# Kernel tuning notes

Measured on AMD Instinct MI355X. Metric: run time of the kernel, lower is better.

## Reference

```python
import jax, jax.numpy as jnp
import numpy as np
from jax import lax

ANCHOR_SCALES = (64.0, 128.0, 256.0)
ANCHOR_RATIOS = (0.5, 1.0, 2.0)
STRIDE = 32
NMS_THRESH = 0.7


def make_anchors(feat_h, feat_w):
    base = []
    for s in ANCHOR_SCALES:
        for r in ANCHOR_RATIOS:
            w = s * np.sqrt(max(r, 1e-6))
            h = s / np.sqrt(max(r, 1e-6))
            base.append([-w / 2, -h / 2, w / 2, h / 2])
    base = jnp.asarray(base, jnp.float32)  # [A=9, 4]
    sx = jnp.arange(feat_w, dtype=jnp.float32) * STRIDE
    sy = jnp.arange(feat_h, dtype=jnp.float32) * STRIDE
    yy, xx = jnp.meshgrid(sy, sx, indexing='ij')
    shifts = jnp.stack([xx, yy, xx, yy], axis=2).reshape(-1, 4)  # [H*W, 4]
    # location-major, anchor-minor -> matches permute(0,2,3,1).view(B,-1,·)
    return (base[None, :, :] + shifts[:, None, :]).reshape(-1, 4)  # [N, 4]


def apply_deltas(anchors, deltas):
    w = anchors[:, 2] - anchors[:, 0]
    h = anchors[:, 3] - anchors[:, 1]
    cx = anchors[:, 0] + 0.5 * w
    cy = anchors[:, 1] + 0.5 * h
    pcx = deltas[:, 0] * w + cx
    pcy = deltas[:, 1] * h + cy
    pw = jnp.exp(deltas[:, 2]) * w
    ph = jnp.exp(deltas[:, 3]) * h
    return jnp.stack([pcx - 0.5 * pw, pcy - 0.5 * ph,
                      pcx + 0.5 * pw, pcy + 0.5 * ph], axis=1)


def pairwise_iou(b):
    area = (b[:, 2] - b[:, 0]) * (b[:, 3] - b[:, 1])
    lt = jnp.maximum(b[:, None, :2], b[None, :, :2])
    rb = jnp.minimum(b[:, None, 2:], b[None, :, 2:])
    wh = jnp.clip(rb - lt, 0.0)
    inter = wh[..., 0] * wh[..., 1]
    return inter / (area[:, None] + area[None, :] - inter)


def nms_keep(boxes, scores, thresh):
    # greedy NMS (torchvision semantics: suppress iou > thresh), returns bool keep mask
    n = boxes.shape[0]
    order = jnp.argsort(-scores)
    sb = boxes[order]
    idx = jnp.arange(n)
    sup_mat = (pairwise_iou(sb) > thresh) & (idx[None, :] > idx[:, None])

    def body(i, sup):
        return sup | ((~sup[i]) & sup_mat[i])

    sup = lax.fori_loop(0, n, body, jnp.zeros(n, bool))
    return jnp.zeros(n, bool).at[order].set(~sup)


def setup_inputs() -> dict:
    key = jax.random.key(0)
    ks = jax.random.split(key, 4)
    features = jax.random.normal(ks[0], (4, 512, 25, 25), jnp.float32)
    conv_w = jax.random.normal(ks[1], (512, 512, 3, 3), jnp.float32) * 0.01
    conv_b = jnp.zeros((512,), jnp.float32)
    cls_w = jax.random.normal(ks[2], (18, 512), jnp.float32) * 0.01
    cls_b = jnp.zeros((18,), jnp.float32)
    bbox_w = jax.random.normal(ks[3], (36, 512), jnp.float32) * 0.01
    bbox_b = jnp.zeros((36,), jnp.float32)
    return {"features": features, "conv_w": conv_w, "conv_b": conv_b,
            "cls_w": cls_w, "cls_b": cls_b, "bbox_w": bbox_w, "bbox_b": bbox_b,
            "img_h": 800, "img_w": 800}


def reference(features, conv_w, conv_b, cls_w, cls_b, bbox_w, bbox_b, img_h, img_w):
    B, _, H, W = features.shape
    x = lax.conv_general_dilated(features, conv_w, (1, 1), 'SAME',
                                 dimension_numbers=('NCHW', 'OIHW', 'NCHW'))
    x = jax.nn.relu(x + conv_b[None, :, None, None])
    obj = jnp.einsum('bchw,oc->bohw', x, cls_w) + cls_b[None, :, None, None]
    dlt = jnp.einsum('bchw,oc->bohw', x, bbox_w) + bbox_b[None, :, None, None]
    obj = obj.transpose(0, 2, 3, 1).reshape(B, -1, 2)      # [B, N, 2]
    dlt = dlt.transpose(0, 2, 3, 1).reshape(B, -1, 4)      # [B, N, 4]

    anchors = make_anchors(H, W)                            # [N, 4]
    props = jax.vmap(lambda d: apply_deltas(anchors, d))(dlt)
    hi = jnp.asarray([img_w, img_h, img_w, img_h], jnp.float32)
    props = jnp.clip(props, 0.0, hi)                        # clip to image
    scores = jax.nn.softmax(obj, axis=-1)[..., 1]           # [B, N]
    keep = jax.vmap(lambda b, s: nms_keep(b, s, NMS_THRESH))(props, scores)
    # suppressed boxes zeroed (fixed-shape analogue of props[keep])
    return props * keep[..., None].astype(props.dtype)
```

## Files before the change

kernel.cpp:

```cpp
#include <hip/hip_runtime.h>


#define NBATCH 4
#define HWDIM  25
#define NPOS   625
#define NM     2500
#define CIN    512
#define NANCH  5625
#define NW     88
#define CAP    4096

typedef unsigned long long u64;
typedef unsigned int u32;

struct BaseAnchors { float x1[9], y1[9], x2[9], y2[9]; };

__device__ __forceinline__ u64 bcast64(u64 v, int lane) {
  unsigned int lo = (unsigned int)v;
  unsigned int hi = (unsigned int)(v >> 32);
  lo = (unsigned int)__builtin_amdgcn_readlane((int)lo, lane);
  hi = (unsigned int)__builtin_amdgcn_readlane((int)hi, lane);
  return (((u64)hi) << 32) | (u64)lo;
}

__device__ __forceinline__ u64 waveOr64(u64 x) {
  unsigned int lo = (unsigned int)x, hi = (unsigned int)(x >> 32);
#pragma unroll
  for (int off = 32; off > 0; off >>= 1) {
    lo |= (unsigned int)__shfl_xor((int)lo, off, 64);
    hi |= (unsigned int)__shfl_xor((int)hi, off, 64);
  }
  return (((u64)hi) << 32) | (u64)lo;
}


__global__ void transpose_features(const float* __restrict__ f, float* __restrict__ fm) {
  __shared__ float tile[32][33];
  int b  = blockIdx.z;
  int p0 = blockIdx.x * 32;
  int c0 = blockIdx.y * 32;
  int tx = threadIdx.x, ty = threadIdx.y;
#pragma unroll
  for (int j = 0; j < 4; j++) {
    int c = c0 + ty + j * 8;
    int p = p0 + tx;
    if (p < NPOS) tile[ty + j * 8][tx] = f[((size_t)(b * CIN + c)) * NPOS + p];
  }
  __syncthreads();
#pragma unroll
  for (int j = 0; j < 4; j++) {
    int p = p0 + ty + j * 8;
    int c = c0 + tx;
    if (p < NPOS) fm[((size_t)(b * NPOS + p)) * CIN + c] = tile[tx][ty + j * 8];
  }
}

__global__ __launch_bounds__(256) void transpose_weights(const float* __restrict__ cw,
                                                         float* __restrict__ Wt) {
  __shared__ float tile[32][289];
  int o0 = blockIdx.x * 32, c0 = blockIdx.y * 32;
  int tid = threadIdx.x;
#pragma unroll
  for (int j = 0; j < 36; j++) {
    int idx = tid + j * 256;
    int o = idx / 288, kk = idx % 288;
    tile[o][kk] = cw[((size_t)(o0 + o)) * 4608 + c0 * 9 + kk];
  }
  __syncthreads();
  int ol = tid & 31, pg = tid >> 5;
#pragma unroll
  for (int j = 0; j < 36; j++) {
    int pair = pg + j * 8;
    int c = pair / 9, tap = pair % 9;
    Wt[((size_t)tap * CIN + (c0 + c)) * 512 + o0 + ol] = tile[ol][pair];
  }
}

__global__ void build_wco(const float* __restrict__ clsw, const float* __restrict__ clsb,
                          const float* __restrict__ bw, const float* __restrict__ bbb,
                          float* __restrict__ Wco, float* __restrict__ bco) {
  int idx = blockIdx.x * 256 + threadIdx.x;
  if (idx < 512 * 64) {
    int c = idx >> 6, o = idx & 63;
    float v = 0.f;
    if (o < 18) v = clsw[o * 512 + c];
    else if (o < 54) v = bw[(o - 18) * 512 + c];
    Wco[idx] = v;
  }
  if (idx < 64) {
    float v = 0.f;
    if (idx < 18) v = clsb[idx];
    else if (idx < 54) v = bbb[idx - 18];
    bco[idx] = v;
  }
}

__global__ void zero_cnt(u32* __restrict__ cnt) {
  int i = blockIdx.x * 64 + threadIdx.x;
  if (i < NBATCH * NW) cnt[i] = 0u;
}

__global__ __launch_bounds__(256) void conv_gemm(const float* __restrict__ fm,
                                                 const float* __restrict__ Wt,
                                                 float* __restrict__ xp) {
  __shared__ __align__(16) float At[32][68];
  __shared__ __align__(16) float Bt[32][64];
  int tid = threadIdx.x;
  int m0 = blockIdx.x << 6;
  int o0 = blockIdx.y << 6;
  int part = blockIdx.z;
  int ti = tid >> 4, tj = tid & 15;
  int si = tid >> 2, sq = tid & 3;
  int skk = tid >> 3, sr = tid & 7;
  float acc[4][4] = {{0.f}};

  int m = m0 + si;
  bool mv = m < NM;
  int mm = mv ? m : 0;
  int bb = mm / NPOS, rem = mm % NPOS;
  int hh = rem / HWDIM, ww = rem % HWDIM;
  int dy = part - 1;

  for (int tt = 0; tt < 3; tt++) {
    int tap = part * 3 + tt;
    int dx = tt - 1;
    int h2 = hh + dy, w2 = ww + dx;
    bool av = mv && ((unsigned)h2 < (unsigned)HWDIM) && ((unsigned)w2 < (unsigned)HWDIM);
    const float* arow = fm + (((size_t)(bb * NPOS + h2 * HWDIM + w2)) << 9);
    const float* bbase = Wt + (((size_t)tap) << 18) + o0;

    float4 a0 = make_float4(0.f, 0.f, 0.f, 0.f), a1 = a0;
    if (av) {
      a0 = *(const float4*)(arow + (sq << 2));
      a1 = *(const float4*)(arow + 16 + (sq << 2));
    }
    const float* bp0 = bbase + (((size_t)skk) << 9);
    float4 b0 = *(const float4*)(bp0 + (sr << 2));
    float4 b1 = *(const float4*)(bp0 + 32 + (sr << 2));

    for (int c0 = 0; c0 < CIN; c0 += 32) {
      __syncthreads();
      int kb = sq << 2;
      At[kb + 0][si] = a0.x; At[kb + 1][si] = a0.y; At[kb + 2][si] = a0.z; At[kb + 3][si] = a0.w;
      At[kb + 16][si] = a1.x; At[kb + 17][si] = a1.y; At[kb + 18][si] = a1.z; At[kb + 19][si] = a1.w;
      *(float4*)&Bt[skk][sr << 2] = b0;
      *(float4*)&Bt[skk][32 + (sr << 2)] = b1;
      float4 na0 = make_float4(0.f, 0.f, 0.f, 0.f), na1 = na0;
      float4 nb0 = na0, nb1 = na0;
      int c1 = c0 + 32;
      if (c1 < CIN) {
        if (av) {
          na0 = *(const float4*)(arow + c1 + (sq << 2));
          na1 = *(const float4*)(arow + c1 + 16 + (sq << 2));
        }
        const float* bp = bbase + (((size_t)(c1 + skk)) << 9);
        nb0 = *(const float4*)(bp + (sr << 2));
        nb1 = *(const float4*)(bp + 32 + (sr << 2));
      }
      __syncthreads();
#pragma unroll
      for (int kk = 0; kk < 32; kk++) {
        float4 avv = *(const float4*)&At[kk][ti << 2];
        float4 bvv = *(const float4*)&Bt[kk][tj << 2];
        float a_[4] = {avv.x, avv.y, avv.z, avv.w};
        float b_[4] = {bvv.x, bvv.y, bvv.z, bvv.w};
#pragma unroll
        for (int u = 0; u < 4; u++)
#pragma unroll
          for (int v = 0; v < 4; v++) acc[u][v] += a_[u] * b_[v];
      }
      a0 = na0; a1 = na1; b0 = nb0; b1 = nb1;
    }
  }
  float* outp = xp + (size_t)part * (NM * 512);
#pragma unroll
  for (int u = 0; u < 4; u++) {
    int mr = m0 + (ti << 2) + u;
    if (mr < NM) {
      float4 r = make_float4(acc[u][0], acc[u][1], acc[u][2], acc[u][3]);
      *(float4*)(outp + (((size_t)mr) << 9) + o0 + (tj << 2)) = r;
    }
  }
}

__global__ void combine_relu(const float* __restrict__ xp, const float* __restrict__ bias,
                             float* __restrict__ x2) {
  int i4 = blockIdx.x * 256 + threadIdx.x;
  if (i4 >= NM * 128) return;
  float4 p0 = *(const float4*)(xp + (size_t)i4 * 4);
  float4 p1 = *(const float4*)(xp + (size_t)(NM * 512) + (size_t)i4 * 4);
  float4 p2 = *(const float4*)(xp + (size_t)(2 * NM * 512) + (size_t)i4 * 4);
  float4 bb = *(const float4*)(bias + (i4 & 127) * 4);
  float4 r;
  r.x = fmaxf(p0.x + p1.x + p2.x + bb.x, 0.f);
  r.y = fmaxf(p0.y + p1.y + p2.y + bb.y, 0.f);
  r.z = fmaxf(p0.z + p1.z + p2.z + bb.z, 0.f);
  r.w = fmaxf(p0.w + p1.w + p2.w + bb.w, 0.f);
  *(float4*)(x2 + (size_t)i4 * 4) = r;
}

__global__ __launch_bounds__(256) void gemm1x1(const float* __restrict__ x2,
                                               const float* __restrict__ Wco,
                                               const float* __restrict__ bco,
                                               float* __restrict__ logits) {
  __shared__ __align__(16) float At[32][68];
  __shared__ __align__(16) float Bt[32][64];
  int tid = threadIdx.x;
  int m0 = blockIdx.x << 6;
  int ti = tid >> 4, tj = tid & 15;
  int si = tid >> 2, sq = tid & 3;
  int skk = tid >> 3, sr = tid & 7;
  float acc[4][4] = {{0.f}};
  int m = m0 + si;
  bool mv = m < NM;
  const float* arow = x2 + (((size_t)(mv ? m : 0)) << 9);
  for (int c0 = 0; c0 < CIN; c0 += 32) {
    __syncthreads();
    float4 a0 = make_float4(0.f, 0.f, 0.f, 0.f), a1 = a0;
    if (mv) {
      a0 = *(const float4*)(arow + c0 + (sq << 2));
      a1 = *(const float4*)(arow + c0 + 16 + (sq << 2));
    }
    int kb = sq << 2;
    At[kb + 0][si] = a0.x; At[kb + 1][si] = a0.y; At[kb + 2][si] = a0.z; At[kb + 3][si] = a0.w;
    At[kb + 16][si] = a1.x; At[kb + 17][si] = a1.y; At[kb + 18][si] = a1.z; At[kb + 19][si] = a1.w;
    const float* bp = Wco + (size_t)(c0 + skk) * 64;
    *(float4*)&Bt[skk][sr << 2] = *(const float4*)(bp + (sr << 2));
    *(float4*)&Bt[skk][32 + (sr << 2)] = *(const float4*)(bp + 32 + (sr << 2));
    __syncthreads();
#pragma unroll
    for (int kk = 0; kk < 32; kk++) {
      float4 avv = *(const float4*)&At[kk][ti << 2];
      float4 bvv = *(const float4*)&Bt[kk][tj << 2];
      float a_[4] = {avv.x, avv.y, avv.z, avv.w};
      float b_[4] = {bvv.x, bvv.y, bvv.z, bvv.w};
#pragma unroll
      for (int u = 0; u < 4; u++)
#pragma unroll
        for (int v = 0; v < 4; v++) acc[u][v] += a_[u] * b_[v];
    }
  }
  float4 bias = *(const float4*)(bco + (tj << 2));
#pragma unroll
  for (int u = 0; u < 4; u++) {
    int mr = m0 + (ti << 2) + u;
    if (mr < NM) {
      float4 r = make_float4(acc[u][0] + bias.x, acc[u][1] + bias.y, acc[u][2] + bias.z,
                             acc[u][3] + bias.w);
      *(float4*)(logits + (size_t)mr * 64 + (tj << 2)) = r;
    }
  }
}

__global__ __launch_bounds__(256) void score_box_kernel(const float* __restrict__ logits,
                                                        const int* __restrict__ ih,
                                                        const int* __restrict__ iw,
                                                        BaseAnchors ba,
                                                        float* __restrict__ scores,
                                                        float* __restrict__ props) {
#pragma clang fp contract(off)
  int n = blockIdx.x * 256 + threadIdx.x;
  if (n >= NBATCH * NANCH) return;
  int b = n / NANCH;
  int r = n % NANCH;
  int pos = r / 9, aa = r % 9;
  int py = pos / HWDIM, px = pos % HWDIM;
  const float* L = logits + (size_t)(b * NPOS + pos) * 64;
  float l0 = L[2 * aa], l1 = L[2 * aa + 1];
  float mx = fmaxf(l0, l1);
  float e0 = expf(l0 - mx), e1 = expf(l1 - mx);
  float s = e1 / (e0 + e1);
  float d0 = L[18 + 4 * aa + 0], d1 = L[18 + 4 * aa + 1];
  float d2 = L[18 + 4 * aa + 2], d3 = L[18 + 4 * aa + 3];
  float xf = (float)px * 32.f, yf = (float)py * 32.f;
  float ax1 = ba.x1[aa] + xf, ay1 = ba.y1[aa] + yf;
  float ax2 = ba.x2[aa] + xf, ay2 = ba.y2[aa] + yf;
  float wA = ax2 - ax1, hA = ay2 - ay1;
  float cx = ax1 + 0.5f * wA, cy = ay1 + 0.5f * hA;
  float pcx = d0 * wA + cx, pcy = d1 * hA + cy;
  float pw = expf(d2) * wA, ph = expf(d3) * hA;
  float x1 = pcx - 0.5f * pw, y1 = pcy - 0.5f * ph;
  float x2 = pcx + 0.5f * pw, y2 = pcy + 0.5f * ph;
  float W = (float)iw[0], H = (float)ih[0];
  x1 = fminf(fmaxf(x1, 0.f), W);
  y1 = fminf(fmaxf(y1, 0.f), H);
  x2 = fminf(fmaxf(x2, 0.f), W);
  y2 = fminf(fmaxf(y2, 0.f), H);
  scores[n] = s;
  *(float4*)(props + (size_t)n * 4) = make_float4(x1, y1, x2, y2);
}

__global__ __launch_bounds__(1024) void sort_kernel(const float* __restrict__ scores,
                                                    const float* __restrict__ props,
                                                    int* __restrict__ order,
                                                    float* __restrict__ sb) {
  __shared__ u64 keys[8192];
  int b = blockIdx.x, tid = threadIdx.x;
  const float* sc = scores + (size_t)b * NANCH;
  for (int i = tid; i < 8192; i += 1024) {
    u64 k = 0ull;
    if (i < NANCH) {
      unsigned int sbits = __float_as_uint(sc[i]);
      k = (((u64)sbits) << 32) | (u64)(~(unsigned int)i);
    }
    keys[i] = k;
  }
  __syncthreads();
  for (int k = 2; k <= 8192; k <<= 1) {
    for (int j = k >> 1; j > 0; j >>= 1) {
#pragma unroll
      for (int s = 0; s < 8; s++) {
        int i = tid + (s << 10);
        int p = i ^ j;
        if (p > i) {
          u64 a = keys[i], c = keys[p];
          bool up = ((i & k) == 0);
          bool sw = up ? (a < c) : (a > c);
          if (sw) { keys[i] = c; keys[p] = a; }
        }
      }
      __syncthreads();
    }
  }
  for (int i = tid; i < NANCH; i += 1024) {
    u64 kk = keys[i];
    int orig = (int)(~(unsigned int)kk);
    order[b * NANCH + i] = orig;
    float4 p = *(const float4*)(props + ((size_t)b * NANCH + orig) * 4);
    *(float4*)(sb + ((size_t)b * NANCH + i) * 4) = p;
  }
}

__global__ __launch_bounds__(64) void nms_mask_kernel(const float* __restrict__ sb,
                                                      uint4* __restrict__ lists,
                                                      u32* __restrict__ cnt,
                                                      u64* __restrict__ maskd) {
#pragma clang fp contract(off)
  int rb = blockIdx.x, cb = blockIdx.y, b = blockIdx.z;
  if (cb < rb) return;
  int lane = threadIdx.x;
  __shared__ float4 cbox[64];
  int j0 = cb << 6;
  const float* sbb = sb + (size_t)b * NANCH * 4;
  if (j0 + lane < NANCH) cbox[lane] = *(const float4*)(sbb + (size_t)(j0 + lane) * 4);
  __syncthreads();
  int i = (rb << 6) + lane;
  if (i >= NANCH) return;
  float4 rbox = *(const float4*)(sbb + (size_t)i * 4);
  float rarea = (rbox.z - rbox.x) * (rbox.w - rbox.y);
  u64 bits = 0ull;
  int jmax = NANCH - j0;
  if (jmax > 64) jmax = 64;
  for (int l = 0; l < jmax; l++) {
    int j = j0 + l;
    if (j > i) {
      float4 c = cbox[l];
      float carea = (c.z - c.x) * (c.w - c.y);
      float ltx = fmaxf(rbox.x, c.x), lty = fmaxf(rbox.y, c.y);
      float rbx = fminf(rbox.z, c.z), rby = fminf(rbox.w, c.w);
      float wx = fmaxf(rbx - ltx, 0.f);
      float wy = fmaxf(rby - lty, 0.f);
      float inter = wx * wy;
      float iou = inter / (rarea + carea - inter);
      if (iou > 0.7f) bits |= (1ull << l);
    }
  }
  if (rb == cb) {
    maskd[((size_t)b * NW + rb) * 64 + lane] = bits;
  } else if (bits) {
    u32 idx = atomicAdd(&cnt[b * NW + cb], 1u);
    if (idx < CAP)
      lists[((size_t)(b * NW + cb)) * CAP + idx] =
          make_uint4((u32)bits, (u32)(bits >> 32), (u32)i, 0u);
  }
}

__global__ __launch_bounds__(64, 1) void nms_scan_kernel(const uint4* __restrict__ lists,
                                                         const u32* __restrict__ cnt,
                                                         const u64* __restrict__ maskd,
                                                         const int* __restrict__ order,
                                                         const float* __restrict__ sb,
                                                         float* __restrict__ out) {
  int b = blockIdx.x;
  int lane = threadIdx.x;
  __shared__ u64 keep_sh[NW];
  const u64* md = maskd + (size_t)b * NW * 64;
  const uint4* lb = lists + (size_t)b * NW * CAP;

  u32 c0 = (lane < NW) ? cnt[b * NW + lane] : 0u;
  u32 c1 = (lane + 64 < NW) ? cnt[b * NW + lane + 64] : 0u;

  u64 diag = md[lane];
  uint4 pf = lb[lane];
  for (int s = 0; s < NW; s++) {
    u64 Mw = diag;
    uint4 e0 = pf;
    if (s + 1 < NW) {
      diag = md[((s + 1) << 6) + lane];
      pf = lb[(size_t)(s + 1) * CAP + lane];
    }

    int cn = (int)(u32)__builtin_amdgcn_readlane(
        (int)((s < 64) ? c0 : c1), (s < 64) ? s : s - 64);
    if (cn > CAP) cn = CAP;

    u64 acc = 0ull;
    if (lane < cn) {
      u64 kw = keep_sh[e0.z >> 6];
      if ((kw >> (e0.z & 63)) & 1ull) acc |= (((u64)e0.y) << 32) | (u64)e0.x;
    }
    for (int p = lane + 64; p < cn; p += 64) {
      uint4 e = lb[(size_t)s * CAP + p];
      u64 kw = keep_sh[e.z >> 6];
      if ((kw >> (e.z & 63)) & 1ull) acc |= (((u64)e.y) << 32) | (u64)e.x;
    }
    u64 cur = waveOr64(acc);

    int nrows = NANCH - (s << 6);
    if (nrows > 64) nrows = 64;
    u64 valid = (nrows < 64) ? ((1ull << nrows) - 1ull) : ~0ull;

    u64 nz = __ballot(Mw != 0ull);
    u64 todo = nz & ~cur & valid;
    while (todo) {
      int t = (int)__builtin_ctzll(todo);
      cur |= bcast64(Mw, t);
      todo &= ~cur;
      todo &= ~(1ull << t);
    }
    u64 alive = (~cur) & valid;
    if (lane == 0) keep_sh[s] = alive;
  }

  for (int i = lane; i < NANCH; i += 64) {
    u64 kw = keep_sh[i >> 6];
    bool kept = ((kw >> (i & 63)) & 1ull) != 0ull;
    int orig = order[b * NANCH + i];
    float4 p = *(const float4*)(sb + ((size_t)b * NANCH + i) * 4);
    float4 o = kept ? p : make_float4(0.f, 0.f, 0.f, 0.f);
    *(float4*)(out + ((size_t)b * NANCH + orig) * 4) = o;
  }
}


extern "C" void kernel_launch(void* const* d_in, const int* in_sizes, int n_in,
                              void* d_out, int out_size, void* d_ws, size_t ws_size,
                              hipStream_t stream) {
  const float* features = (const float*)d_in[0];
  const float* conv_w   = (const float*)d_in[1];
  const float* conv_b   = (const float*)d_in[2];
  const float* cls_w    = (const float*)d_in[3];
  const float* cls_b    = (const float*)d_in[4];
  const float* bbox_w   = (const float*)d_in[5];
  const float* bbox_b   = (const float*)d_in[6];
  const int*   img_h    = (const int*)d_in[7];
  const int*   img_w    = (const int*)d_in[8];
  float* out = (float*)d_out;
  char* ws = (char*)d_ws;

  const size_t OFF_FM    = 0;
  const size_t OFF_WT    = 5120000;
  const size_t OFF_XP    = 14557184;
  const size_t OFF_LISTS = 0;
  const size_t OFF_CNT   = 23068672;
  const size_t OFF_MASKD = 23070208;
  const size_t OFF_X2  = 29917184;
  const size_t OFF_WCO = 35037184;
  const size_t OFF_BCO = 35168256;
  const size_t OFF_LOG = 35168512;
  const size_t OFF_SC  = 35808512;
  const size_t OFF_PR  = 35898512;
  const size_t OFF_ORD = 36258512;
  const size_t OFF_SB  = 36348512;
  const size_t WS_NEEDED = 36708512;
  if (ws_size < WS_NEEDED) return;

  float* fm   = (float*)(ws + OFF_FM);
  float* Wt   = (float*)(ws + OFF_WT);
  float* xp   = (float*)(ws + OFF_XP);
  uint4* lists = (uint4*)(ws + OFF_LISTS);
  u32*   cnt   = (u32*)(ws + OFF_CNT);
  u64*   maskd = (u64*)(ws + OFF_MASKD);
  float* x2   = (float*)(ws + OFF_X2);
  float* Wco  = (float*)(ws + OFF_WCO);
  float* bco  = (float*)(ws + OFF_BCO);
  float* logits = (float*)(ws + OFF_LOG);
  float* scores = (float*)(ws + OFF_SC);
  float* props  = (float*)(ws + OFF_PR);
  int*   order  = (int*)(ws + OFF_ORD);
  float* sb     = (float*)(ws + OFF_SB);

  BaseAnchors ba;
  {
    const double scales[3] = {64.0, 128.0, 256.0};
    const double ratios[3] = {0.5, 1.0, 2.0};
    int a = 0;
    for (int si = 0; si < 3; si++)
      for (int ri = 0; ri < 3; ri++, a++) {
        double w = scales[si] * sqrt(ratios[ri]);
        double h = scales[si] / sqrt(ratios[ri]);
        ba.x1[a] = (float)(-w / 2.0);
        ba.y1[a] = (float)(-h / 2.0);
        ba.x2[a] = (float)(w / 2.0);
        ba.y2[a] = (float)(h / 2.0);
      }
  }

  transpose_features<<<dim3(20, 16, 4), dim3(32, 8), 0, stream>>>(features, fm);
  transpose_weights<<<dim3(16, 16), 256, 0, stream>>>(conv_w, Wt);
  build_wco<<<128, 256, 0, stream>>>(cls_w, cls_b, bbox_w, bbox_b, Wco, bco);
  conv_gemm<<<dim3(40, 8, 3), 256, 0, stream>>>(fm, Wt, xp);
  combine_relu<<<1250, 256, 0, stream>>>(xp, conv_b, x2);
  gemm1x1<<<40, 256, 0, stream>>>(x2, Wco, bco, logits);
  score_box_kernel<<<88, 256, 0, stream>>>(logits, img_h, img_w, ba, scores, props);
  sort_kernel<<<4, 1024, 0, stream>>>(scores, props, order, sb);
  zero_cnt<<<6, 64, 0, stream>>>(cnt);
  nms_mask_kernel<<<dim3(NW, NW, 4), 64, 0, stream>>>(sb, lists, cnt, maskd);
  nms_scan_kernel<<<4, 64, 0, stream>>>(lists, cnt, maskd, order, sb, out);
}
```

Measured before the change: 457.5 us.

## Replace bitonic sort with stable LSD radix sort in shared memory

Swaps the 8192-element 64-bit-key bitonic sort for a 4-pass, 8-bit-digit LSD radix sort over 32-bit score keys with separate index values. Per-wave histograms, a block prefix scan and ballot-based match ranking give a stable descending order, so index tie-breaking is preserved. The goal is to cut the roughly 91 barrier-separated bitonic stages down to a few dozen barriers. In exchange it uses more LDS, which limits occupancy, and adds scan overhead.

Result: faster. 390.0 us (-14.7%).

```diff
diff --git a/kernel.cpp b/kernel.cpp
--- a/kernel.cpp
+++ b/kernel.cpp
@@ -9,6 +9,7 @@
 #define NANCH  5625
 #define NW     88
 #define CAP    4096
+#define SORTN  6144
 
 typedef unsigned long long u64;
 typedef unsigned int u32;
@@ -290,43 +291,89 @@
   *(float4*)(props + (size_t)n * 4) = make_float4(x1, y1, x2, y2);
 }
 
-__global__ __launch_bounds__(1024) void sort_kernel(const float* __restrict__ scores,
-                                                    const float* __restrict__ props,
-                                                    int* __restrict__ order,
-                                                    float* __restrict__ sb) {
-  __shared__ u64 keys[8192];
+__global__ __launch_bounds__(1024, 1) void radix_sort_kernel(const float* __restrict__ scores,
+                                                             const float* __restrict__ props,
+                                                             int* __restrict__ order,
+                                                             float* __restrict__ sb) {
+  __shared__ u32 kA[SORTN], vA[SORTN], kB[SORTN], vB[SORTN];
+  __shared__ u32 hist[16][256];
+  __shared__ u32 tot[256], base[256], tmp[256];
   int b = blockIdx.x, tid = threadIdx.x;
+  int lane = tid & 63, wv = tid >> 6;
   const float* sc = scores + (size_t)b * NANCH;
-  for (int i = tid; i < 8192; i += 1024) {
-    u64 k = 0ull;
-    if (i < NANCH) {
-      unsigned int sbits = __float_as_uint(sc[i]);
-      k = (((u64)sbits) << 32) | (u64)(~(unsigned int)i);
-    }
-    keys[i] = k;
+
+  for (int i = tid; i < SORTN; i += 1024) {
+    kA[i] = (i < NANCH) ? __float_as_uint(sc[i]) : 0u;
+    vA[i] = (u32)i;
   }
   __syncthreads();
-  for (int k = 2; k <= 8192; k <<= 1) {
-    for (int j = k >> 1; j > 0; j >>= 1) {
-#pragma unroll
-      for (int s = 0; s < 8; s++) {
-        int i = tid + (s << 10);
-        int p = i ^ j;
-        if (p > i) {
-          u64 a = keys[i], c = keys[p];
-          bool up = ((i & k) == 0);
-          bool sw = up ? (a < c) : (a > c);
-          if (sw) { keys[i] = c; keys[p] = a; }
-        }
+
+  for (int pass = 0; pass < 4; pass++) {
+    int shift = pass << 3;
+    u32* ks = (pass & 1) ? kB : kA;
+    u32* vs = (pass & 1) ? vB : vA;
+    u32* kd = (pass & 1) ? kA : kB;
+    u32* vd = (pass & 1) ? vA : vB;
+    for (int i = tid; i < 4096; i += 1024) ((u32*)hist)[i] = 0u;
+    __syncthreads();
+    for (int r = 0; r < 6; r++) {
+      int i = wv * 384 + (r << 6) + lane;
+      u32 d = 255u - ((ks[i] >> shift) & 255u);
+      atomicAdd(&hist[wv][d], 1u);
+    }
+    __syncthreads();
+    if (tid < 256) {
+      u32 run = 0;
+#pragma unroll
+      for (int w = 0; w < 16; w++) { u32 t = hist[w][tid]; hist[w][tid] = run; run += t; }
+      tot[tid] = run;
+    }
+    __syncthreads();
+    if (tid < 256) tmp[tid] = tot[tid];
+    __syncthreads();
+    for (int off = 1; off < 256; off <<= 1) {
+      u32 v = 0;
+      if (tid < 256 && tid >= off) v = tmp[tid - off];
+      __syncthreads();
+      if (tid < 256) tmp[tid] += v;
+      __syncthreads();
+    }
+    if (tid < 256) base[tid] = tmp[tid] - tot[tid];
+    __syncthreads();
+    if (tid < 256) {
+      u32 bs = base[tid];
+#pragma unroll
+      for (int w = 0; w < 16; w++) hist[w][tid] += bs;
+    }
+    __syncthreads();
+    for (int r = 0; r < 6; r++) {
+      int i = wv * 384 + (r << 6) + lane;
+      u32 key = ks[i], val = vs[i];
+      u32 d = 255u - ((key >> shift) & 255u);
+      u64 grp = ~0ull;
+#pragma unroll
+      for (int bit = 0; bit < 8; bit++) {
+        u64 bal = __ballot(((d >> bit) & 1u) != 0u);
+        grp &= ((d >> bit) & 1u) ? bal : ~bal;
       }
-      __syncthreads();
-    }
-  }
+      u64 ltmask = (1ull << lane) - 1ull;
+      u32 rank = (u32)__popcll(grp & ltmask);
+      int leader = (int)__builtin_ctzll(grp);
+      u32 oldv = 0;
+      if (lane == leader) oldv = atomicAdd(&hist[wv][d], (u32)__popcll(grp));
+      oldv = (u32)__shfl((int)oldv, leader, 64);
+      u32 slot = oldv + rank;
+      kd[slot] = key;
+      vd[slot] = val;
+    }
+    __syncthreads();
+  }
+
+  const float* pr = props + (size_t)b * NANCH * 4;
   for (int i = tid; i < NANCH; i += 1024) {
-    u64 kk = keys[i];
-    int orig = (int)(~(unsigned int)kk);
-    order[b * NANCH + i] = orig;
-    float4 p = *(const float4*)(props + ((size_t)b * NANCH + orig) * 4);
+    u32 orig = vA[i];
+    order[b * NANCH + i] = (int)orig;
+    float4 p = *(const float4*)(pr + (size_t)orig * 4);
     *(float4*)(sb + ((size_t)b * NANCH + i) * 4) = p;
   }
 }
@@ -513,7 +560,7 @@
   combine_relu<<<1250, 256, 0, stream>>>(xp, conv_b, x2);
   gemm1x1<<<40, 256, 0, stream>>>(x2, Wco, bco, logits);
   score_box_kernel<<<88, 256, 0, stream>>>(logits, img_h, img_w, ba, scores, props);
-  sort_kernel<<<4, 1024, 0, stream>>>(scores, props, order, sb);
+  radix_sort_kernel<<<4, 1024, 0, stream>>>(scores, props, order, sb);
   zero_cnt<<<6, 64, 0, stream>>>(cnt);
   nms_mask_kernel<<<dim3(NW, NW, 4), 64, 0, stream>>>(sb, lists, cnt, maskd);
   nms_scan_kernel<<<4, 64, 0, stream>>>(lists, cnt, maskd, order, sb, out);
```
